# Optimization experiments

Hardware: AMD Instinct MI355X
Metric: run time of the kernel (lower is better)

Reference implementation:

```python
import jax, jax.numpy as jnp
import numpy as np

N_SRC, N_DST, E = 65536, 16384, 262144
IN, HID, H = 256, 128, 4
N_POI, K = 100000, 50
NEG_SLOPE = 0.2


def setup_inputs() -> dict:
    key = jax.random.key(0)
    ks = jax.random.split(key, 13)
    feat = jax.random.normal(ks[0], (N_SRC, IN), jnp.float32)
    poi_cat_feat = jax.random.normal(ks[1], (N_POI, IN), jnp.float32)
    poi_coeff = jax.random.uniform(ks[2], (N_POI, K), jnp.float32)
    fc_w = jax.random.normal(ks[3], (H * HID, IN), jnp.float32) * 0.05
    attn_l = jax.random.normal(ks[4], (H, HID), jnp.float32) * 0.05
    attn_r = jax.random.normal(ks[5], (H, HID), jnp.float32) * 0.05
    bias_p = jnp.zeros((H * HID,), jnp.float32)
    res_w = jax.random.normal(ks[6], (H * HID, IN), jnp.float32) * 0.05
    w_w = jax.random.normal(ks[7], (HID, IN), jnp.float32) * 0.05
    src_idx = jax.random.randint(ks[8], (E,), 0, N_SRC)
    dst_idx = jax.random.randint(ks[9], (E,), 0, N_DST)
    output_nodes = jax.random.randint(ks[10], (N_DST,), 0, N_POI)
    neighbor_counts = jax.random.randint(ks[11], (N_POI,), 1, K + 1)
    return dict(feat=feat, poi_cat_feat=poi_cat_feat, poi_coeff=poi_coeff,
                fc_w=fc_w, attn_l=attn_l, attn_r=attn_r, bias_p=bias_p,
                res_w=res_w, w_w=w_w, src_idx=src_idx, dst_idx=dst_idx,
                output_nodes=output_nodes, neighbor_counts=neighbor_counts)


def reference(feat, poi_cat_feat, poi_coeff, fc_w, attn_l, attn_r, bias_p,
              res_w, w_w, src_idx, dst_idx, output_nodes, neighbor_counts):
    # ---- DGL GATConv on block (src -> dst), feat_drop/attn_drop = 0 (eval) ----
    feat_src = (feat @ fc_w.T).reshape(N_SRC, H, HID)        # [Nsrc,H,D]
    el = jnp.einsum('nhd,hd->nh', feat_src, attn_l)          # [Nsrc,H]
    er = jnp.einsum('nhd,hd->nh', feat_src[:N_DST], attn_r)  # [Ndst,H]
    e = jax.nn.leaky_relu(el[src_idx] + er[dst_idx], NEG_SLOPE)  # [E,H]
    # edge softmax per destination node (numerically stable)
    m = jax.ops.segment_max(e, dst_idx, num_segments=N_DST)
    m = jnp.where(jnp.isfinite(m), m, 0.0)
    ex = jnp.exp(e - m[dst_idx])
    denom = jax.ops.segment_sum(ex, dst_idx, num_segments=N_DST)
    a = ex / jnp.maximum(denom[dst_idx], 1e-9)               # [E,H]
    msgs = a[:, :, None] * feat_src[src_idx]                 # [E,H,D]
    rst = jax.ops.segment_sum(msgs, dst_idx, num_segments=N_DST)  # [Ndst,H,D]
    res = (feat[:N_DST] @ res_w.T).reshape(N_DST, H, HID)    # residual projection
    feat_gat = jax.nn.elu(rst + res + bias_p.reshape(1, H, HID))
    # ---- per-node neighbor-weighted sum: sum_j beta[nid,j] * W @ poi_cat_feat[nid],
    #      over first min(count,50) neighbors (cap-50 padded mask) ----
    cf = poi_cat_feat[output_nodes]                          # [Ndst,IN]
    valid = (jnp.arange(K)[None, :] < neighbor_counts[output_nodes][:, None])
    s = jnp.sum(poi_coeff[output_nodes] * valid.astype(cf.dtype), axis=-1)  # [Ndst]
    feat_dist = (cf @ w_w.T) * s[:, None]                    # [Ndst,HID]
    out = jax.nn.relu((feat_gat + feat_dist[:, None, :]) / 2)
    return out
```

## Files before the change

kernel.cpp:

```cpp
#include <hip/hip_runtime.h>
#include <hip/hip_cooperative_groups.h>

namespace cgrp = cooperative_groups;

#define N_SRC 65536
#define N_DST 16384
#define NEDGE 262144
#define FIN 256
#define HID 128
#define KNB 50
#define NEG 0.2f
#define BCAP 64

typedef short bf8 __attribute__((ext_vector_type(8)));
typedef float f32x4 __attribute__((ext_vector_type(4)));

static __device__ __forceinline__ short f2bf(float f) {
    union { float f; unsigned u; } v; v.f = f;
    unsigned r = v.u + 0x7fffu + ((v.u >> 16) & 1u);
    return (short)(r >> 16);
}
static __device__ __forceinline__ float bf2f(short b) {
    union { unsigned u; float f; } v; v.u = ((unsigned)(unsigned short)b) << 16;
    return v.f;
}

static __device__ __forceinline__ unsigned char f2e4(float f) {
    union { float f; unsigned u; } v; v.f = f;
    unsigned s = (v.u >> 24) & 0x80u;
    v.u &= 0x7FFFFFFFu;
    v.f = fminf(v.f, 240.0f);
    unsigned u = v.u + 0x00080000u;
    int eb = (int)(u >> 23) - 120;
    if (eb < 1) return (unsigned char)s;
    unsigned m = (u >> 20) & 7u;
    return (unsigned char)(s | ((unsigned)eb << 3) | m);
}

struct MegaP {
    const float *feat, *poi, *coeff, *attnl, *attnr, *bias;
    const float *fc32, *rw32, *ww32;
    const int *src, *dst, *nodes, *ncnt;
    short *feat_bf, *fcw, *resw, *ww, *cf;
    unsigned char *fsrc8;
    short *res, *fdist;
    float *el, *er, *sArr, *out;
    int *counts, *bucket;
};


static __device__ __forceinline__ void dev_prep(int vb, int t, const MegaP& P) {
    if (vb < 16384) {
        int i = vb * 256 + t;
        float4 v = ((const float4*)P.feat)[i];
        short4 o; o.x = f2bf(v.x); o.y = f2bf(v.y); o.z = f2bf(v.z); o.w = f2bf(v.w);
        ((short4*)P.feat_bf)[i] = o;
    } else if (vb < 16672) {
        int i = (vb - 16384) * 256 + t;
        const float* src; short* dst; int off;
        if (i < 32768) { src = P.fc32; dst = P.fcw; off = i; }
        else if (i < 65536) { src = P.rw32; dst = P.resw; off = i - 32768; }
        else { src = P.ww32; dst = P.ww; off = i - 65536; }
        float4 v = ((const float4*)src)[off];
        short4 o; o.x = f2bf(v.x); o.y = f2bf(v.y); o.z = f2bf(v.z); o.w = f2bf(v.w);
        ((short4*)dst)[off] = o;
    } else if (vb < 20768) {
        int wv = t >> 6, lane = t & 63;
        int row = (vb - 16672) * 4 + wv;
        int nid = P.nodes[row];
        float4 v = ((const float4*)(P.poi + (size_t)nid * FIN))[lane];
        short4 o; o.x = f2bf(v.x); o.y = f2bf(v.y); o.z = f2bf(v.z); o.w = f2bf(v.w);
        ((short4*)(P.cf + (size_t)row * FIN))[lane] = o;
        int cnt = P.ncnt[nid];
        float s = (lane < cnt && lane < KNB) ? P.coeff[(size_t)nid * KNB + lane] : 0.f;
        for (int m = 1; m < 64; m <<= 1) s += __shfl_xor(s, m);
        if (lane == 0) P.sArr[row] = s;
    } else {
        int e = (vb - 20768) * 256 + t;
        int d = P.dst[e];
        int pos = atomicAdd(&P.counts[d], 1);
        if (pos < BCAP) P.bucket[d * BCAP + pos] = P.src[e];
    }
}

static __device__ __forceinline__ void dev_gemm_tile(
    int b, int t, const MegaP& P, short* Abuf, short* Bbuf) {
    const short *A, *W; const float* scale = nullptr;
    short* C16 = nullptr;
    int N = 512, do_elr = 0, rowBase, colBase;
    if (b < 2048) {
        A = P.feat_bf; W = P.fcw; do_elr = 1;
        colBase = (b & 3) * 128; rowBase = (b >> 2) * 128;
    } else if (b < 2560) {
        int bb = b - 2048;
        A = P.feat_bf; W = P.resw; C16 = P.res;
        colBase = (bb & 3) * 128; rowBase = (bb >> 2) * 128;
    } else {
        int bb = b - 2560;
        A = P.cf; W = P.ww; C16 = P.fdist; scale = P.sArr; N = 128;
        colBase = 0; rowBase = bb * 128;
    }
    int wv = t >> 6, lane = t & 63;
    int l15 = lane & 15, quad = lane >> 4;
    int s0 = (wv & 1) * 8;
    int rsub = lane >> 3;
    int cgn = (lane & 7) ^ rsub;
    const short* sbase = (wv < 2) ? (A + (size_t)rowBase * FIN)
                                  : (W + (size_t)colBase * FIN);
    short* dbase = (wv < 2) ? Abuf : Bbuf;

    f32x4 acc[2][8] = {};
    for (int kb = 0; kb < 4; kb++) {
#pragma unroll
        for (int q = 0; q < 8; q++) {
            int slab = s0 + q;
            int r_loc = slab * 8 + rsub;
            __builtin_amdgcn_global_load_lds(
                (const __attribute__((address_space(1))) void*)(sbase + (size_t)r_loc * FIN + kb * 64 + cgn * 8),
                (__attribute__((address_space(3))) void*)(dbase + slab * 512), 16, 0, 0);
        }
        asm volatile("s_waitcnt vmcnt(0)" ::: "memory");
        __syncthreads();
#pragma unroll
        for (int kk = 0; kk < 2; kk++) {
            int gidx = (quad + kk * 4) ^ (l15 & 7);
            bf8 a[2], bfr[8];
#pragma unroll
            for (int i = 0; i < 2; i++) {
                int row = wv * 32 + i * 16 + l15;
                a[i] = *(const bf8*)(Abuf + (row * 8 + gidx) * 8);
            }
#pragma unroll
            for (int j = 0; j < 8; j++) {
                int row = j * 16 + l15;
                bfr[j] = *(const bf8*)(Bbuf + (row * 8 + gidx) * 8);
            }
#pragma unroll
            for (int i = 0; i < 2; i++)
#pragma unroll
                for (int j = 0; j < 8; j++)
                    acc[i][j] = __builtin_amdgcn_mfma_f32_16x16x32_bf16(a[i], bfr[j], acc[i][j], 0, 0, 0);
        }
        if (kb < 3) __syncthreads();
    }
#pragma unroll
    for (int i = 0; i < 2; i++)
#pragma unroll
        for (int r = 0; r < 4; r++) {
            int row = rowBase + wv * 32 + i * 16 + quad * 4 + r;
            if (do_elr) {
#pragma unroll
                for (int j = 0; j < 8; j++)
                    P.fsrc8[(size_t)row * 512 + colBase + j * 16 + l15] = f2e4(acc[i][j][r]);
            } else {
                float sc = scale ? scale[row] : 1.0f;
#pragma unroll
                for (int j = 0; j < 8; j++)
                    C16[(size_t)row * N + colBase + j * 16 + l15] = f2bf(acc[i][j][r] * sc);
            }
        }
    if (do_elr) {
        int h = colBase >> 7;
        float alv[8], arv[8];
#pragma unroll
        for (int j = 0; j < 8; j++) {
            alv[j] = P.attnl[h * HID + j * 16 + l15];
            arv[j] = P.attnr[h * HID + j * 16 + l15];
        }
#pragma unroll
        for (int i = 0; i < 2; i++)
#pragma unroll
            for (int r = 0; r < 4; r++) {
                float dl = 0.f, dr = 0.f;
#pragma unroll
                for (int j = 0; j < 8; j++) {
                    float c = acc[i][j][r];
                    dl += c * alv[j];
                    dr += c * arv[j];
                }
                dl += __shfl_xor(dl, 1); dr += __shfl_xor(dr, 1);
                dl += __shfl_xor(dl, 2); dr += __shfl_xor(dr, 2);
                dl += __shfl_xor(dl, 4); dr += __shfl_xor(dr, 4);
                dl += __shfl_xor(dl, 8); dr += __shfl_xor(dr, 8);
                if (l15 == 0) {
                    int row = rowBase + wv * 32 + i * 16 + quad * 4 + r;
                    P.el[row * 4 + h] = dl;
                    if (row < N_DST) P.er[row * 4 + h] = dr;
                }
            }
    }
}

static __device__ __forceinline__ void dev_agg_one(
    int d, int lane, const MegaP& P, float* aW, int* sW) {
    int cnt = P.counts[d]; cnt = cnt < BCAP ? cnt : BCAP;
    float4 erv = *(const float4*)(P.er + (size_t)d * 4);

    int srow = 0;
    float v0 = -1e30f, v1 = -1e30f, v2 = -1e30f, v3 = -1e30f;
    if (lane < cnt) {
        srow = P.bucket[d * BCAP + lane];
        float4 lv = *(const float4*)(P.el + (size_t)srow * 4);
        v0 = lv.x + erv.x; v0 = v0 > 0 ? v0 : NEG * v0;
        v1 = lv.y + erv.y; v1 = v1 > 0 ? v1 : NEG * v1;
        v2 = lv.z + erv.z; v2 = v2 > 0 ? v2 : NEG * v2;
        v3 = lv.w + erv.w; v3 = v3 > 0 ? v3 : NEG * v3;
    }
    float m0 = v0, m1 = v1, m2 = v2, m3 = v3;
    for (int sh = 1; sh < 64; sh <<= 1) {
        m0 = fmaxf(m0, __shfl_xor(m0, sh)); m1 = fmaxf(m1, __shfl_xor(m1, sh));
        m2 = fmaxf(m2, __shfl_xor(m2, sh)); m3 = fmaxf(m3, __shfl_xor(m3, sh));
    }
    float e0 = 0.f, e1 = 0.f, e2 = 0.f, e3 = 0.f;
    if (lane < cnt) {
        e0 = __expf(v0 - m0); e1 = __expf(v1 - m1);
        e2 = __expf(v2 - m2); e3 = __expf(v3 - m3);
    }
    float s0 = e0, s1 = e1, s2 = e2, s3 = e3;
    for (int sh = 1; sh < 64; sh <<= 1) {
        s0 += __shfl_xor(s0, sh); s1 += __shfl_xor(s1, sh);
        s2 += __shfl_xor(s2, sh); s3 += __shfl_xor(s3, sh);
    }
    const float S = 0x1p120f;
    float i0 = S / fmaxf(s0, 1e-9f), i1 = S / fmaxf(s1, 1e-9f);
    float i2 = S / fmaxf(s2, 1e-9f), i3 = S / fmaxf(s3, 1e-9f);
    *(float4*)&aW[lane * 4] = make_float4(e0 * i0, e1 * i1, e2 * i2, e3 * i3);
    sW[lane] = srow;
    asm volatile("s_waitcnt lgkmcnt(0)" ::: "memory");

    int myh = lane >> 4, col0 = lane * 8;
    float acc[8] = {0.f, 0.f, 0.f, 0.f, 0.f, 0.f, 0.f, 0.f};
    for (int c = 0; c < cnt; c++) {
        int srw = sW[c];
        float afs = aW[c * 4 + myh];
        const unsigned char* p = P.fsrc8 + ((size_t)srw << 9) + col0;
        uint2 w8 = *(const uint2*)p;
#pragma unroll
        for (int j = 0; j < 4; j++) {
            unsigned blo = (w8.x >> (8 * j)) & 0xFFu;
            unsigned bhi = (w8.y >> (8 * j)) & 0xFFu;
            union { unsigned u; float f; } xl, xh;
            xl.u = ((blo & 0x80u) << 24) | ((blo & 0x7Fu) << 20);
            xh.u = ((bhi & 0x80u) << 24) | ((bhi & 0x7Fu) << 20);
            acc[j]     = fmaf(afs, xl.f, acc[j]);
            acc[j + 4] = fmaf(afs, xh.f, acc[j + 4]);
        }
    }

    bf8 rv = *(const bf8*)(P.res + (size_t)d * 512 + col0);
    float4 bv0 = *(const float4*)(P.bias + col0);
    float4 bv1 = *(const float4*)(P.bias + col0 + 4);
    float bb[8] = {bv0.x, bv0.y, bv0.z, bv0.w, bv1.x, bv1.y, bv1.z, bv1.w};
    bf8 fv = *(const bf8*)(P.fdist + (size_t)d * HID + (col0 & 127));
    float o[8];
#pragma unroll
    for (int j = 0; j < 8; j++) {
        float g = acc[j] + bf2f(rv[j]) + bb[j];
        g = g > 0 ? g : expm1f(g);
        float v = (g + bf2f(fv[j])) * 0.5f;
        o[j] = v > 0 ? v : 0.f;
    }
    float* op = P.out + (size_t)d * 512 + col0;
    *(float4*)op = make_float4(o[0], o[1], o[2], o[3]);
    *(float4*)(op + 4) = make_float4(o[4], o[5], o[6], o[7]);
}

__global__ __launch_bounds__(256, 3) void k_mega(MegaP P) {
    __shared__ __align__(16) char smem[32768];
    cgrp::grid_group grid = cgrp::this_grid();
    int t = threadIdx.x;
    int nb = gridDim.x;

    for (int i = blockIdx.x * 256 + t; i < N_DST; i += nb * 256)
        P.counts[i] = 0;
    grid.sync();

    for (int vb = blockIdx.x; vb < 21792; vb += nb)
        dev_prep(vb, t, P);
    grid.sync();

    {
        short* Abuf = (short*)smem;
        short* Bbuf = (short*)(smem + 16384);
        int xcd = blockIdx.x & 7, lix = blockIdx.x >> 3, nw = nb >> 3;
        for (int ti = lix; ti < 336; ti += nw) {
            dev_gemm_tile(xcd * 336 + ti, t, P, Abuf, Bbuf);
            __syncthreads();
        }
    }
    grid.sync();

    {
        float* aSm = (float*)smem;
        int* sSm = (int*)(smem + 4096);
        int wv = t >> 6, lane = t & 63;
        float* aW = aSm + wv * 256;
        int* sW = sSm + wv * 64;
        for (int d = blockIdx.x * 4 + wv; d < N_DST; d += nb * 4)
            dev_agg_one(d, lane, P, aW, sW);
    }
}

__global__ __launch_bounds__(256) void k_prep(MegaP P) {
    dev_prep(blockIdx.x, threadIdx.x, P);
}
__global__ __launch_bounds__(256, 3) void k_gemm(MegaP P) {
    __shared__ __align__(16) short Abuf[128 * 64];
    __shared__ __align__(16) short Bbuf[128 * 64];
    int b0 = blockIdx.x;
    dev_gemm_tile((b0 & 7) * 336 + (b0 >> 3), threadIdx.x, P, Abuf, Bbuf);
}
__global__ __launch_bounds__(256) void k_agg2(MegaP P) {
    __shared__ __align__(16) float aSm[4][256];
    __shared__ int sSm[4][64];
    int wv = threadIdx.x >> 6, lane = threadIdx.x & 63;
    dev_agg_one(blockIdx.x * 4 + wv, lane, P, aSm[wv], sSm[wv]);
}

extern "C" void kernel_launch(void* const* d_in, const int* in_sizes, int n_in,
                              void* d_out, int out_size, void* d_ws, size_t ws_size,
                              hipStream_t stream) {
    char* w = (char*)d_ws;
    auto alloc = [&](size_t bytes) -> char* {
        char* p = w; w += (bytes + 255) & ~(size_t)255; return p;
    };
    MegaP P;
    P.feat  = (const float*)d_in[0];
    P.poi   = (const float*)d_in[1];
    P.coeff = (const float*)d_in[2];
    P.fc32  = (const float*)d_in[3];
    P.attnl = (const float*)d_in[4];
    P.attnr = (const float*)d_in[5];
    P.bias  = (const float*)d_in[6];
    P.rw32  = (const float*)d_in[7];
    P.ww32  = (const float*)d_in[8];
    P.src   = (const int*)d_in[9];
    P.dst   = (const int*)d_in[10];
    P.nodes = (const int*)d_in[11];
    P.ncnt  = (const int*)d_in[12];
    P.out   = (float*)d_out;

    P.feat_bf = (short*)alloc((size_t)N_SRC * FIN * 2);
    P.fcw     = (short*)alloc((size_t)512 * FIN * 2);
    P.resw    = (short*)alloc((size_t)512 * FIN * 2);
    P.ww      = (short*)alloc((size_t)HID * FIN * 2);
    P.cf      = (short*)alloc((size_t)N_DST * FIN * 2);
    P.fsrc8   = (unsigned char*)alloc((size_t)N_SRC * 512);
    P.res     = (short*)alloc((size_t)N_DST * 512 * 2);
    P.fdist   = (short*)alloc((size_t)N_DST * HID * 2);
    P.el      = (float*)alloc((size_t)N_SRC * 4 * 4);
    P.er      = (float*)alloc((size_t)N_DST * 4 * 4);
    P.sArr    = (float*)alloc((size_t)N_DST * 4);
    P.counts  = (int*)alloc((size_t)N_DST * 4);
    P.bucket  = (int*)alloc((size_t)N_DST * BCAP * 4);

    int maxb = 0;
    hipError_t qrc = hipOccupancyMaxActiveBlocksPerMultiprocessor(
        &maxb, (const void*)k_mega, 256, 0);
    if (qrc == hipSuccess && maxb >= 2) {
        int bpc = maxb < 3 ? maxb : 3;
        dim3 grid(256 * bpc);
        void* args[] = { (void*)&P };
        hipError_t rc = hipLaunchCooperativeKernel((const void*)k_mega, grid,
                                                   dim3(256), args, 0, stream);
        if (rc == hipSuccess) return;
    }

    hipMemsetAsync(P.counts, 0, N_DST * 4, stream);
    k_prep<<<21792, 256, 0, stream>>>(P);
    k_gemm<<<2688, 256, 0, stream>>>(P);
    k_agg2<<<N_DST / 4, 256, 0, stream>>>(P);
}
```

Baseline: 305.3 us.

## Fuse fp32-to-bf16 feature conversion into GEMM, stage epilogue via LDS, drop cooperative kernel

Removes the separate pass that converted the 64 MB feat matrix to bf16. The GEMM now loads fp32 feat directly and converts it in registers while filling LDS, which avoids a full write and reread of a bf16 copy. The GEMM epilogue now stages output tiles in swizzled LDS and writes them with coalesced 16-byte stores instead of scattered byte and short stores. The cooperative mega-kernel with grid syncs is replaced by three plain launches. The trade-off is that A-tile loads no longer use async global-to-LDS copies, and each feat row is read in fp32 by four column tiles.

```diff
diff --git a/kernel.cpp b/kernel.cpp
--- a/kernel.cpp
+++ b/kernel.cpp
@@ -1,7 +1,4 @@
 #include <hip/hip_runtime.h>
-#include <hip/hip_cooperative_groups.h>
-
-namespace cgrp = cooperative_groups;
 
 #define N_SRC 65536
 #define N_DST 16384
@@ -41,22 +38,17 @@
     const float *feat, *poi, *coeff, *attnl, *attnr, *bias;
     const float *fc32, *rw32, *ww32;
     const int *src, *dst, *nodes, *ncnt;
-    short *feat_bf, *fcw, *resw, *ww, *cf;
+    short *fcw, *resw, *ww, *cf;
     unsigned char *fsrc8;
     short *res, *fdist;
     float *el, *er, *sArr, *out;
     int *counts, *bucket;
 };
 
-
-static __device__ __forceinline__ void dev_prep(int vb, int t, const MegaP& P) {
-    if (vb < 16384) {
+__global__ __launch_bounds__(256) void k_prep(MegaP P) {
+    int vb = blockIdx.x, t = threadIdx.x;
+    if (vb < 288) {
         int i = vb * 256 + t;
-        float4 v = ((const float4*)P.feat)[i];
-        short4 o; o.x = f2bf(v.x); o.y = f2bf(v.y); o.z = f2bf(v.z); o.w = f2bf(v.w);
-        ((short4*)P.feat_bf)[i] = o;
-    } else if (vb < 16672) {
-        int i = (vb - 16384) * 256 + t;
         const float* src; short* dst; int off;
         if (i < 32768) { src = P.fc32; dst = P.fcw; off = i; }
         else if (i < 65536) { src = P.rw32; dst = P.resw; off = i - 32768; }
@@ -64,9 +56,9 @@
         float4 v = ((const float4*)src)[off];
         short4 o; o.x = f2bf(v.x); o.y = f2bf(v.y); o.z = f2bf(v.z); o.w = f2bf(v.w);
         ((short4*)dst)[off] = o;
-    } else if (vb < 20768) {
+    } else if (vb < 4384) {
         int wv = t >> 6, lane = t & 63;
-        int row = (vb - 16672) * 4 + wv;
+        int row = (vb - 288) * 4 + wv;
         int nid = P.nodes[row];
         float4 v = ((const float4*)(P.poi + (size_t)nid * FIN))[lane];
         short4 o; o.x = f2bf(v.x); o.y = f2bf(v.y); o.z = f2bf(v.z); o.w = f2bf(v.w);
@@ -76,48 +68,80 @@
         for (int m = 1; m < 64; m <<= 1) s += __shfl_xor(s, m);
         if (lane == 0) P.sArr[row] = s;
     } else {
-        int e = (vb - 20768) * 256 + t;
+        int e = (vb - 4384) * 256 + t;
         int d = P.dst[e];
         int pos = atomicAdd(&P.counts[d], 1);
         if (pos < BCAP) P.bucket[d * BCAP + pos] = P.src[e];
     }
 }
 
-static __device__ __forceinline__ void dev_gemm_tile(
-    int b, int t, const MegaP& P, short* Abuf, short* Bbuf) {
-    const short *A, *W; const float* scale = nullptr;
+__global__ __launch_bounds__(256, 3) void k_gemm(MegaP P) {
+    __shared__ __align__(16) short SM[16384];
+    short* Abuf = SM;
+    short* Bbuf = SM + 8192;
+    int b0 = blockIdx.x;
+    int b = (b0 & 7) * 336 + (b0 >> 3);
+    const short* W; const float* scale = nullptr;
     short* C16 = nullptr;
-    int N = 512, do_elr = 0, rowBase, colBase;
+    int N = 512, do_elr = 0, a_f32 = 0, rowBase, colBase;
     if (b < 2048) {
-        A = P.feat_bf; W = P.fcw; do_elr = 1;
+        W = P.fcw; do_elr = 1; a_f32 = 1;
         colBase = (b & 3) * 128; rowBase = (b >> 2) * 128;
     } else if (b < 2560) {
         int bb = b - 2048;
-        A = P.feat_bf; W = P.resw; C16 = P.res;
+        W = P.resw; C16 = P.res; a_f32 = 1;
         colBase = (bb & 3) * 128; rowBase = (bb >> 2) * 128;
     } else {
         int bb = b - 2560;
-        A = P.cf; W = P.ww; C16 = P.fdist; scale = P.sArr; N = 128;
+        W = P.ww; C16 = P.fdist; scale = P.sArr; N = 128;
         colBase = 0; rowBase = bb * 128;
     }
-    int wv = t >> 6, lane = t & 63;
+    int t = threadIdx.x, wv = t >> 6, lane = t & 63;
     int l15 = lane & 15, quad = lane >> 4;
     int s0 = (wv & 1) * 8;
     int rsub = lane >> 3;
-    int cgn = (lane & 7) ^ rsub;
-    const short* sbase = (wv < 2) ? (A + (size_t)rowBase * FIN)
-                                  : (W + (size_t)colBase * FIN);
-    short* dbase = (wv < 2) ? Abuf : Bbuf;
+    int cg = (lane & 7) ^ rsub;
+    const short* wbase = W + (size_t)colBase * FIN;
+    const float* abase32 = P.feat + (size_t)rowBase * FIN;
+    const short* abase16 = P.cf + (size_t)rowBase * FIN;
 
     f32x4 acc[2][8] = {};
     for (int kb = 0; kb < 4; kb++) {
-#pragma unroll
-        for (int q = 0; q < 8; q++) {
-            int slab = s0 + q;
-            int r_loc = slab * 8 + rsub;
-            __builtin_amdgcn_global_load_lds(
-                (const __attribute__((address_space(1))) void*)(sbase + (size_t)r_loc * FIN + kb * 64 + cgn * 8),
-                (__attribute__((address_space(3))) void*)(dbase + slab * 512), 16, 0, 0);
+        if (wv < 2) {
+            if (a_f32) {
+#pragma unroll
+                for (int q = 0; q < 8; q++) {
+                    int slab = s0 + q;
+                    int r_loc = slab * 8 + rsub;
+                    const float* fp = abase32 + (size_t)r_loc * FIN + kb * 64 + cg * 8;
+                    float4 u0 = *(const float4*)fp;
+                    float4 u1 = *(const float4*)(fp + 4);
+                    bf8 o;
+                    o[0] = f2bf(u0.x); o[1] = f2bf(u0.y);
+                    o[2] = f2bf(u0.z); o[3] = f2bf(u0.w);
+                    o[4] = f2bf(u1.x); o[5] = f2bf(u1.y);
+                    o[6] = f2bf(u1.z); o[7] = f2bf(u1.w);
+                    *(bf8*)(Abuf + slab * 512 + lane * 8) = o;
+                }
+            } else {
+#pragma unroll
+                for (int q = 0; q < 8; q++) {
+                    int slab = s0 + q;
+                    int r_loc = slab * 8 + rsub;
+                    __builtin_amdgcn_global_load_lds(
+                        (const __attribute__((address_space(1))) void*)(abase16 + (size_t)r_loc * FIN + kb * 64 + cg * 8),
+                        (__attribute__((address_space(3))) void*)(Abuf + slab * 512), 16, 0, 0);
+                }
+            }
+        } else {
+#pragma unroll
+            for (int q = 0; q < 8; q++) {
+                int slab = s0 + q;
+                int r_loc = slab * 8 + rsub;
+                __builtin_amdgcn_global_load_lds(
+                    (const __attribute__((address_space(1))) void*)(wbase + (size_t)r_loc * FIN + kb * 64 + cg * 8),
+                    (__attribute__((address_space(3))) void*)(Bbuf + slab * 512), 16, 0, 0);
+            }
         }
         asm volatile("s_waitcnt vmcnt(0)" ::: "memory");
         __syncthreads();
@@ -143,56 +167,90 @@
         }
         if (kb < 3) __syncthreads();
     }
-#pragma unroll
-    for (int i = 0; i < 2; i++)
-#pragma unroll
-        for (int r = 0; r < 4; r++) {
-            int row = rowBase + wv * 32 + i * 16 + quad * 4 + r;
-            if (do_elr) {
+    __syncthreads();
+
+    if (do_elr) {
+        unsigned char* SMb = (unsigned char*)SM;
+#pragma unroll
+        for (int i = 0; i < 2; i++)
+#pragma unroll
+            for (int r = 0; r < 4; r++) {
+                int row = wv * 32 + i * 16 + quad * 4 + r;
+                int xr = (row & 7) << 4;
 #pragma unroll
                 for (int j = 0; j < 8; j++)
-                    P.fsrc8[(size_t)row * 512 + colBase + j * 16 + l15] = f2e4(acc[i][j][r]);
-            } else {
-                float sc = scale ? scale[row] : 1.0f;
+                    SMb[row * 128 + ((j * 16 + l15) ^ xr)] = f2e4(acc[i][j][r]);
+            }
+        {
+            int h = colBase >> 7;
+            float alv[8], arv[8];
+#pragma unroll
+            for (int j = 0; j < 8; j++) {
+                alv[j] = P.attnl[h * HID + j * 16 + l15];
+                arv[j] = P.attnr[h * HID + j * 16 + l15];
+            }
+#pragma unroll
+            for (int i = 0; i < 2; i++)
+#pragma unroll
+                for (int r = 0; r < 4; r++) {
+                    float dl = 0.f, dr = 0.f;
+#pragma unroll
+                    for (int j = 0; j < 8; j++) {
+                        float c = acc[i][j][r];
+                        dl += c * alv[j];
+                        dr += c * arv[j];
+                    }
+                    dl += __shfl_xor(dl, 1); dr += __shfl_xor(dr, 1);
+                    dl += __shfl_xor(dl, 2); dr += __shfl_xor(dr, 2);
+                    dl += __shfl_xor(dl, 4); dr += __shfl_xor(dr, 4);
+                    dl += __shfl_xor(dl, 8); dr += __shfl_xor(dr, 8);
+                    if (l15 == 0) {
+                        int row = rowBase + wv * 32 + i * 16 + quad * 4 + r;
+                        P.el[row * 4 + h] = dl;
+                        if (row < N_DST) P.er[row * 4 + h] = dr;
+                    }
+                }
+        }
+        __syncthreads();
+        int row = t >> 1, h2 = (t & 1) * 64;
+        int xr = (row & 7) << 4;
+        unsigned char* dp = P.fsrc8 + (size_t)(rowBase + row) * 512 + colBase + h2;
+#pragma unroll
+        for (int k = 0; k < 4; k++) {
+            uint4 v = *(const uint4*)(SMb + row * 128 + ((h2 + k * 16) ^ xr));
+            *(uint4*)(dp + k * 16) = v;
+        }
+    } else {
+#pragma unroll
+        for (int i = 0; i < 2; i++)
+#pragma unroll
+            for (int r = 0; r < 4; r++) {
+                int row = wv * 32 + i * 16 + quad * 4 + r;
+                float sc = scale ? scale[rowBase + row] : 1.0f;
+                int xr = (row & 7) << 4;
 #pragma unroll
                 for (int j = 0; j < 8; j++)
-                    C16[(size_t)row * N + colBase + j * 16 + l15] = f2bf(acc[i][j][r] * sc);
-            }
-        }
-    if (do_elr) {
-        int h = colBase >> 7;
-        float alv[8], arv[8];
-#pragma unroll
-        for (int j = 0; j < 8; j++) {
-            alv[j] = P.attnl[h * HID + j * 16 + l15];
-            arv[j] = P.attnr[h * HID + j * 16 + l15];
-        }
-#pragma unroll
-        for (int i = 0; i < 2; i++)
-#pragma unroll
-            for (int r = 0; r < 4; r++) {
-                float dl = 0.f, dr = 0.f;
-#pragma unroll
-                for (int j = 0; j < 8; j++) {
-                    float c = acc[i][j][r];
-                    dl += c * alv[j];
-                    dr += c * arv[j];
-                }
-                dl += __shfl_xor(dl, 1); dr += __shfl_xor(dr, 1);
-                dl += __shfl_xor(dl, 2); dr += __shfl_xor(dr, 2);
-                dl += __shfl_xor(dl, 4); dr += __shfl_xor(dr, 4);
-                dl += __shfl_xor(dl, 8); dr += __shfl_xor(dr, 8);
-                if (l15 == 0) {
-                    int row = rowBase + wv * 32 + i * 16 + quad * 4 + r;
-                    P.el[row * 4 + h] = dl;
-                    if (row < N_DST) P.er[row * 4 + h] = dr;
-                }
-            }
-    }
-}
-
-static __device__ __forceinline__ void dev_agg_one(
-    int d, int lane, const MegaP& P, float* aW, int* sW) {
+                    SM[row * 128 + ((j * 16 + l15) ^ xr)] = f2bf(acc[i][j][r] * sc);
+            }
+        __syncthreads();
+        int row = t >> 1, h2 = (t & 1) * 64;
+        int xr = (row & 7) << 4;
+        short* dp = C16 + (size_t)(rowBase + row) * N + colBase + h2;
+#pragma unroll
+        for (int k = 0; k < 8; k++) {
+            uint4 v = *(const uint4*)(SM + row * 128 + ((h2 + k * 8) ^ xr));
+            *(uint4*)(dp + k * 8) = v;
+        }
+    }
+}
+
+__global__ __launch_bounds__(256) void k_agg(MegaP P) {
+    __shared__ __align__(16) float aSm[4][256];
+    __shared__ int sSm[4][64];
+    int wv = threadIdx.x >> 6, lane = threadIdx.x & 63;
+    float* aW = aSm[wv];
+    int* sW = sSm[wv];
+    int d = blockIdx.x * 4 + wv;
     int cnt = P.counts[d]; cnt = cnt < BCAP ? cnt : BCAP;
     float4 erv = *(const float4*)(P.er + (size_t)d * 4);
 
@@ -263,58 +321,6 @@
     float* op = P.out + (size_t)d * 512 + col0;
     *(float4*)op = make_float4(o[0], o[1], o[2], o[3]);
     *(float4*)(op + 4) = make_float4(o[4], o[5], o[6], o[7]);
-}
-
-__global__ __launch_bounds__(256, 3) void k_mega(MegaP P) {
-    __shared__ __align__(16) char smem[32768];
-    cgrp::grid_group grid = cgrp::this_grid();
-    int t = threadIdx.x;
-    int nb = gridDim.x;
-
-    for (int i = blockIdx.x * 256 + t; i < N_DST; i += nb * 256)
-        P.counts[i] = 0;
-    grid.sync();
-
-    for (int vb = blockIdx.x; vb < 21792; vb += nb)
-        dev_prep(vb, t, P);
-    grid.sync();
-
-    {
-        short* Abuf = (short*)smem;
-        short* Bbuf = (short*)(smem + 16384);
-        int xcd = blockIdx.x & 7, lix = blockIdx.x >> 3, nw = nb >> 3;
-        for (int ti = lix; ti < 336; ti += nw) {
-            dev_gemm_tile(xcd * 336 + ti, t, P, Abuf, Bbuf);
-            __syncthreads();
-        }
-    }
-    grid.sync();
-
-    {
-        float* aSm = (float*)smem;
-        int* sSm = (int*)(smem + 4096);
-        int wv = t >> 6, lane = t & 63;
-        float* aW = aSm + wv * 256;
-        int* sW = sSm + wv * 64;
-        for (int d = blockIdx.x * 4 + wv; d < N_DST; d += nb * 4)
-            dev_agg_one(d, lane, P, aW, sW);
-    }
-}
-
-__global__ __launch_bounds__(256) void k_prep(MegaP P) {
-    dev_prep(blockIdx.x, threadIdx.x, P);
-}
-__global__ __launch_bounds__(256, 3) void k_gemm(MegaP P) {
-    __shared__ __align__(16) short Abuf[128 * 64];
-    __shared__ __align__(16) short Bbuf[128 * 64];
-    int b0 = blockIdx.x;
-    dev_gemm_tile((b0 & 7) * 336 + (b0 >> 3), threadIdx.x, P, Abuf, Bbuf);
-}
-__global__ __launch_bounds__(256) void k_agg2(MegaP P) {
-    __shared__ __align__(16) float aSm[4][256];
-    __shared__ int sSm[4][64];
-    int wv = threadIdx.x >> 6, lane = threadIdx.x & 63;
-    dev_agg_one(blockIdx.x * 4 + wv, lane, P, aSm[wv], sSm[wv]);
 }
 
 extern "C" void kernel_launch(void* const* d_in, const int* in_sizes, int n_in,
@@ -340,7 +346,6 @@
     P.ncnt  = (const int*)d_in[12];
     P.out   = (float*)d_out;
 
-    P.feat_bf = (short*)alloc((size_t)N_SRC * FIN * 2);
     P.fcw     = (short*)alloc((size_t)512 * FIN * 2);
     P.resw    = (short*)alloc((size_t)512 * FIN * 2);
     P.ww      = (short*)alloc((size_t)HID * FIN * 2);
@@ -354,20 +359,8 @@
     P.counts  = (int*)alloc((size_t)N_DST * 4);
     P.bucket  = (int*)alloc((size_t)N_DST * BCAP * 4);
 
-    int maxb = 0;
-    hipError_t qrc = hipOccupancyMaxActiveBlocksPerMultiprocessor(
-        &maxb, (const void*)k_mega, 256, 0);
-    if (qrc == hipSuccess && maxb >= 2) {
-        int bpc = maxb < 3 ? maxb : 3;
-        dim3 grid(256 * bpc);
-        void* args[] = { (void*)&P };
-        hipError_t rc = hipLaunchCooperativeKernel((const void*)k_mega, grid,
-                                                   dim3(256), args, 0, stream);
-        if (rc == hipSuccess) return;
-    }
-
     hipMemsetAsync(P.counts, 0, N_DST * 4, stream);
-    k_prep<<<21792, 256, 0, stream>>>(P);
+    k_prep<<<5408, 256, 0, stream>>>(P);
     k_gemm<<<2688, 256, 0, stream>>>(P);
-    k_agg2<<<N_DST / 4, 256, 0, stream>>>(P);
-}
+    k_agg<<<N_DST / 4, 256, 0, stream>>>(P);
+}
```

New measurement: 399.2 us. 30.8% more time.
